# Kernel tuning notes

Hardware: AMD Instinct MI355X
Metric: run time of the kernel (lower is better)

Reference implementation:

```python
import jax, jax.numpy as jnp
import numpy as np

N_NODES = 20000
N_EDGES = 320000
IN_CH = 64
OUT_CH = 128

def _gat(x, src, dst, W, a_src, a_dst, bias, concat):
    # PyG GATConv: linear -> per-edge leaky_relu attention logits -> segment softmax over dst -> scatter-weighted sum
    N = x.shape[0]
    H, C = a_src.shape
    xl = (x @ W).reshape(N, H, C)                       # [N,H,C]
    al = (xl * a_src).sum(-1)                           # [N,H] src logits
    ar = (xl * a_dst).sum(-1)                           # [N,H] dst logits
    e = jax.nn.leaky_relu(al[src] + ar[dst], 0.2)       # [E,H]
    emax = jax.ops.segment_max(e, dst, num_segments=N)  # every node has a self loop -> no empty segments
    ee = jnp.exp(e - emax[dst])
    denom = jax.ops.segment_sum(ee, dst, num_segments=N)
    alpha = ee / (denom[dst] + 1e-16)                   # [E,H]
    out = jax.ops.segment_sum(xl[src] * alpha[:, :, None], dst, num_segments=N)  # [N,H,C]
    out = out.reshape(N, H * C) if concat else out.mean(axis=1)
    return out + bias

def setup_inputs() -> dict:
    key = jax.random.key(0)
    ks = jax.random.split(key, 32)
    def lin(k, fi, fo):
        return jax.random.normal(k, (fi, fo), jnp.float32) / np.sqrt(fi)
    def att(k, H, C):
        return jax.random.normal(k, (H, C), jnp.float32) / np.sqrt(C)
    x = jax.random.normal(ks[0], (N_NODES, IN_CH), jnp.float32)
    src = jax.random.randint(ks[1], (N_EDGES,), 0, N_NODES, jnp.int32)
    dst = jax.random.randint(ks[2], (N_EDGES,), 0, N_NODES, jnp.int32)
    dst = jnp.where(dst == src, (dst + 1) % N_NODES, dst)  # avoid pre-existing self loops
    edge_index = jnp.stack([src, dst])
    edge_time = jax.random.uniform(ks[3], (N_EDGES,), jnp.float32)
    H = 4
    return {
        "x": x, "edge_time": edge_time,
        "W1": lin(ks[4], IN_CH, 512), "as1": att(ks[5], H, 128), "ad1": att(ks[6], H, 128), "b1": jnp.zeros((512,), jnp.float32),
        "W2": lin(ks[7], 512, 512),   "as2": att(ks[8], H, 128), "ad2": att(ks[9], H, 128), "b2": jnp.zeros((512,), jnp.float32),
        "W3": lin(ks[10], 512, 512),  "as3": att(ks[11], H, 128), "ad3": att(ks[12], H, 128), "b3": jnp.zeros((OUT_CH,), jnp.float32),
        "tW1": lin(ks[13], 1, 64), "tb1": jnp.zeros((64,), jnp.float32),
        "tW2": lin(ks[14], 64, OUT_CH), "tb2": jnp.zeros((OUT_CH,), jnp.float32),
        "fW1": lin(ks[15], 2 * OUT_CH, OUT_CH), "fb1": jnp.zeros((OUT_CH,), jnp.float32),
        "fW2": lin(ks[16], OUT_CH, OUT_CH), "fb2": jnp.zeros((OUT_CH,), jnp.float32),
        "ln_g": jnp.ones((OUT_CH,), jnp.float32), "ln_b": jnp.zeros((OUT_CH,), jnp.float32),
        "rW": lin(ks[17], IN_CH, OUT_CH), "rb": jnp.zeros((OUT_CH,), jnp.float32),
        "edge_index": edge_index,
    }

def reference(x, edge_time, W1, as1, ad1, b1, W2, as2, ad2, b2, W3, as3, ad3, b3,
              tW1, tb1, tW2, tb2, fW1, fb1, fW2, fb2, ln_g, ln_b, rW, rb, edge_index):
    N = x.shape[0]
    loop = jnp.arange(N, dtype=edge_index.dtype)
    src = jnp.concatenate([edge_index[0], loop])
    dst = jnp.concatenate([edge_index[1], loop])
    # temporal embedding of raw (pre-self-loop) edges
    t = edge_time[:, None]
    time_emb = jax.nn.relu(t @ tW1 + tb1) @ tW2 + tb2    # [E, OUT_CH]
    x_res = x @ rW + rb
    h = jax.nn.relu(_gat(x, src, dst, W1, as1, ad1, b1, True))
    h = jax.nn.relu(_gat(h, src, dst, W2, as2, ad2, b2, True))
    h = jax.nn.relu(_gat(h, src, dst, W3, as3, ad3, b3, False))
    # x_agg[row] += h[col]  with (row, col) = (src, dst) incl. self loops
    agg = jax.ops.segment_sum(h[dst], src, num_segments=N)
    tm = jnp.broadcast_to(time_emb.mean(axis=0)[None, :], (N, time_emb.shape[1]))
    z = jnp.concatenate([agg, tm], axis=1)
    z = jax.nn.relu(z @ fW1 + fb1)                        # dropout is identity in eval
    z = z @ fW2 + fb2
    mu = z.mean(-1, keepdims=True)
    var = ((z - mu) ** 2).mean(-1, keepdims=True)
    z = (z - mu) / jnp.sqrt(var + 1e-5) * ln_g + ln_b
    return z + x_res
```

## Files before the change

kernel.cpp:

```cpp
#include <hip/hip_runtime.h>
#include <hip/hip_bf16.h>
#include <math.h>

typedef short bf16x8 __attribute__((ext_vector_type(8)));
typedef float f32x4 __attribute__((ext_vector_type(4)));

__device__ __forceinline__ float lrelu(float v) { return v > 0.f ? v : 0.2f * v; }

__device__ __forceinline__ void gload16(const void* g, void* l) {
  __builtin_amdgcn_global_load_lds(
      (const __attribute__((address_space(1))) void*)g,
      (__attribute__((address_space(3))) void*)l, 16, 0, 0);
}

__device__ __forceinline__ uint packbf(float v0, float v1) {
  __hip_bfloat16 h0 = __float2bfloat16(v0);
  __hip_bfloat16 h1 = __float2bfloat16(v1);
  return (uint)(*(unsigned short*)&h0) | ((uint)(*(unsigned short*)&h1) << 16);
}

struct PrepArgs {
  const float* W[6]; __hip_bfloat16* Wt[6]; int K[6]; int Nw[6]; int tstart[6];
  int NC, XB;
};

__global__ __launch_bounds__(256) void k_build(
    const int* __restrict__ src, const int* __restrict__ dst, int E,
    int* cntD, int* cntS,
    const float* __restrict__ et, const float* __restrict__ tW1,
    const float* __restrict__ tb1, float* __restrict__ tacc,
    PrepArgs a, const float* __restrict__ x,
    __hip_bfloat16* __restrict__ xbf, __hip_bfloat16* __restrict__ habf,
    __hip_bfloat16* __restrict__ aggbf, int N, int Mp, int EB) {
  __shared__ float se[256];
  __shared__ float buf[256];
  __shared__ float tile[32][65];
  int t = threadIdx.x;
  int bid = blockIdx.x;
  if (bid < EB) {
    int e = bid * 256 + t;
    if (e < E) {
      atomicAdd(&cntD[dst[e]], 1);
      atomicAdd(&cntS[src[e]], 1);
    }
    if (bid < 256) {
      int l = t & 63, w = t >> 6;
      float wk = tW1[l], bk = tb1[l];
      float a0 = 0.f, a1 = 0.f, a2 = 0.f, a3 = 0.f;
      for (int base = bid * 256; base < E; base += 256 * 256) {
        int idx = base + t;
        se[t] = (idx < E) ? et[idx] : 0.f;
        __syncthreads();
        int cnt = E - base; if (cnt > 256) cnt = 256;
        int s0 = w * 64;
        int c = cnt - s0; if (c < 0) c = 0; if (c > 64) c = 64;
        int j = 0;
        for (; j + 4 <= c; j += 4) {
          a0 += fmaxf(se[s0 + j] * wk + bk, 0.f);
          a1 += fmaxf(se[s0 + j + 1] * wk + bk, 0.f);
          a2 += fmaxf(se[s0 + j + 2] * wk + bk, 0.f);
          a3 += fmaxf(se[s0 + j + 3] * wk + bk, 0.f);
        }
        for (; j < c; ++j) a0 += fmaxf(se[s0 + j] * wk + bk, 0.f);
        __syncthreads();
      }
      buf[t] = (a0 + a1) + (a2 + a3);
      __syncthreads();
      if (t < 64) {
        float s = buf[t] + buf[t + 64] + buf[t + 128] + buf[t + 192];
        atomicAdd(&tacc[t], s);
      }
    }
    return;
  }
  int pbid = bid - EB;
  if (pbid < a.NC) {
    int m = 0;
#pragma unroll
    for (int i = 1; i < 6; ++i) if (pbid >= a.tstart[i]) m = i;
    const float* W = a.W[m];
    __hip_bfloat16* Wt = a.Wt[m];
    int K = a.K[m], Nw = a.Nw[m];
    int lt = pbid - a.tstart[m];
    int ntn = Nw >> 6;
    int bk = (lt / ntn) * 32, bn = (lt % ntn) * 64;
    int rn = t & 63, rk = t >> 6;
#pragma unroll
    for (int i = 0; i < 8; ++i)
      tile[rk + i * 4][rn] = W[(size_t)(bk + rk + i * 4) * Nw + bn + rn];
    __syncthreads();
    int wk2 = (t & 15) * 2, wn = t >> 4;
    uint* Wo = (uint*)Wt;
#pragma unroll
    for (int i = 0; i < 4; ++i) {
      int n = wn + i * 16;
      Wo[((size_t)(bn + n) * K + bk + wk2) >> 1] = packbf(tile[wk2][n], tile[wk2 + 1][n]);
    }
  } else if (pbid < a.NC + a.XB) {
    int i4 = (pbid - a.NC) * 256 + t;
    int row = i4 >> 4;
    float4 v = make_float4(0.f, 0.f, 0.f, 0.f);
    if (row < N) v = ((const float4*)x)[i4];
    uint2 p; p.x = packbf(v.x, v.y); p.y = packbf(v.z, v.w);
    ((uint2*)xbf)[i4] = p;
  } else {
    int row = N + (pbid - a.NC - a.XB);
    ((uint*)habf)[(size_t)row * 256 + t] = 0;
    if (t < 64) ((uint*)aggbf)[(size_t)row * 64 + t] = 0;
  }
}

__global__ __launch_bounds__(1024) void k_scan2c(const int* __restrict__ cntD, int* __restrict__ offD,
    const int* __restrict__ cntS, int* __restrict__ offS, int n,
    const float* __restrict__ tacc, const float* __restrict__ tW2,
    const float* __restrict__ tb2, const float* __restrict__ fW1,
    const float* __restrict__ fb1, float* __restrict__ cvec, int E) {
  int t = threadIdx.x;
  if (blockIdx.x == 2) {
    __shared__ float tm[128];
    if (t < 128) {
      float inv = 1.f / (float)E;
      float acc = tb2[t];
      for (int k = 0; k < 64; ++k) acc += (tacc[k] * inv) * tW2[k * 128 + t];
      tm[t] = acc;
    }
    __syncthreads();
    if (t < 128) {
      float c = fb1[t];
      for (int k = 0; k < 128; ++k) c += tm[k] * fW1[(128 + k) * 128 + t];
      cvec[t] = c;
    }
    return;
  }
  const int* cnt = blockIdx.x ? cntS : cntD;
  int* off = blockIdx.x ? offS : offD;
  __shared__ int sums[1024];
  int PT = (n + 1023) >> 10;
  int start = t * PT;
  int local = 0;
  for (int i = 0; i < PT; ++i) {
    int idx = start + i;
    if (idx < n) local += cnt[idx];
  }
  sums[t] = local;
  __syncthreads();
  for (int o = 1; o < 1024; o <<= 1) {
    int v = (t >= o) ? sums[t - o] : 0;
    __syncthreads();
    sums[t] += v;
    __syncthreads();
  }
  int run = sums[t] - local;
  for (int i = 0; i < PT; ++i) {
    int idx = start + i;
    if (idx < n) { off[idx] = run; run += cnt[idx]; }
  }
  if (t == 1023) off[n] = run;
}

__global__ __launch_bounds__(256) void gemm_e1(
    const __hip_bfloat16* __restrict__ A, const __hip_bfloat16* __restrict__ Bt,
    void* __restrict__ Cout, int M, int Nn, int K,
    const float* __restrict__ asrc, const float* __restrict__ adst,
    float* __restrict__ al, float* __restrict__ ar,
    float* __restrict__ C2, const float* __restrict__ bias2,
    int TBx,
    const int* __restrict__ fsrc, const int* __restrict__ fdst, int fE,
    const int* __restrict__ foffD, int* fcurD, int* flstD,
    const int* __restrict__ foffS, int* fcurS, int* flstS)
{
  __shared__ short As0[128 * 32];
  __shared__ short As1[128 * 32];
  __shared__ short Bs0[128 * 32];
  __shared__ short Bs1[128 * 32];
  if ((int)blockIdx.x >= TBx) {
    if (blockIdx.y == 0) {
      int e = ((int)blockIdx.x - TBx) * 256 + (int)threadIdx.x;
      if (e < fE) {
        int d = fdst[e], s = fsrc[e];
        int p = atomicAdd(&fcurD[d], 1);
        flstD[foffD[d] + p] = s;
        int q = atomicAdd(&fcurS[s], 1);
        flstS[foffS[s] + q] = d;
      }
    }
    return;
  }
  int tid = threadIdx.x;
  int bm = blockIdx.x * 128;
  int cb = blockIdx.y;
  int bn = cb * 128;
  int w = tid >> 6, l = tid & 63;
  int wr = (w >> 1) * 64, wc = (w & 1) * 64;
  f32x4 acc[4][4] = {};
  const short* Ag = (const short*)A;
  const short* Bg = (const short*)Bt;

  for (int k0 = 0; k0 < K; k0 += 64) {
#pragma unroll
    for (int i = 0; i < 2; ++i) {
      int slot = i * 256 + tid;
      int row = slot >> 2;
      int col = (slot & 3) * 8;
      const short* Arow = Ag + (size_t)(bm + row) * K + k0 + col;
      const short* Brow = Bg + (size_t)(bn + row) * K + k0 + col;
      gload16(Arow, &As0[slot * 8]);
      gload16(Arow + 32, &As1[slot * 8]);
      gload16(Brow, &Bs0[slot * 8]);
      gload16(Brow + 32, &Bs1[slot * 8]);
    }
    __syncthreads();
    {
      bf16x8 af[4], bfr[4];
#pragma unroll
      for (int m = 0; m < 4; ++m)
        af[m] = *(const bf16x8*)&As0[(wr + m * 16 + (l & 15)) * 32 + (l >> 4) * 8];
#pragma unroll
      for (int n = 0; n < 4; ++n)
        bfr[n] = *(const bf16x8*)&Bs0[(wc + n * 16 + (l & 15)) * 32 + (l >> 4) * 8];
#pragma unroll
      for (int m = 0; m < 4; ++m)
#pragma unroll
        for (int n = 0; n < 4; ++n)
          acc[m][n] = __builtin_amdgcn_mfma_f32_16x16x32_bf16(af[m], bfr[n], acc[m][n], 0, 0, 0);
    }
    {
      bf16x8 af[4], bfr[4];
#pragma unroll
      for (int m = 0; m < 4; ++m)
        af[m] = *(const bf16x8*)&As1[(wr + m * 16 + (l & 15)) * 32 + (l >> 4) * 8];
#pragma unroll
      for (int n = 0; n < 4; ++n)
        bfr[n] = *(const bf16x8*)&Bs1[(wc + n * 16 + (l & 15)) * 32 + (l >> 4) * 8];
#pragma unroll
      for (int m = 0; m < 4; ++m)
#pragma unroll
        for (int n = 0; n < 4; ++n)
          acc[m][n] = __builtin_amdgcn_mfma_f32_16x16x32_bf16(af[m], bfr[n], acc[m][n], 0, 0, 0);
    }
    __syncthreads();
  }

  int g = l >> 4, cc = l & 15, cr = g * 4;

  if (cb < 4) {
#pragma unroll
    for (int n = 0; n < 4; ++n) {
      int col = bn + wc + n * 16 + cc;
#pragma unroll
      for (int m = 0; m < 4; ++m) {
#pragma unroll
        for (int r = 0; r < 4; ++r) {
          int gm = bm + wr + m * 16 + cr + r;
          if (gm < M)
            ((__hip_bfloat16*)Cout)[(size_t)gm * 512 + col] = __float2bfloat16(acc[m][n][r]);
        }
      }
    }
    float asv[4], adv[4];
#pragma unroll
    for (int n = 0; n < 4; ++n) {
      int ch = bn + wc + n * 16 + cc;
      asv[n] = asrc[ch]; adv[n] = adst[ch];
    }
    float* spal = (float*)As0;
    float* spar = spal + 256;
#pragma unroll
    for (int m = 0; m < 4; ++m) {
#pragma unroll
      for (int r = 0; r < 4; ++r) {
        float pa = acc[m][0][r] * asv[0] + acc[m][1][r] * asv[1]
                 + acc[m][2][r] * asv[2] + acc[m][3][r] * asv[3];
        float pb = acc[m][0][r] * adv[0] + acc[m][1][r] * adv[1]
                 + acc[m][2][r] * adv[2] + acc[m][3][r] * adv[3];
#pragma unroll
        for (int o = 1; o < 16; o <<= 1) {
          pa += __shfl_xor(pa, o);
          pb += __shfl_xor(pb, o);
        }
        if (cc == 0) {
          int rl = m * 16 + cr + r;
          spal[w * 64 + rl] = pa;
          spar[w * 64 + rl] = pb;
        }
      }
    }
    __syncthreads();
    if ((w & 1) == 0) {
      float av = spal[w * 64 + l] + spal[(w + 1) * 64 + l];
      float rv = spar[w * 64 + l] + spar[(w + 1) * 64 + l];
      int row = bm + wr + l;
      if (row < Nn) { al[row * 4 + cb] = av; ar[row * 4 + cb] = rv; }
    }
  } else {
#pragma unroll
    for (int n = 0; n < 4; ++n) {
      int col2 = wc + n * 16 + cc;
      float bb = bias2[col2];
#pragma unroll
      for (int m = 0; m < 4; ++m) {
#pragma unroll
        for (int r = 0; r < 4; ++r) {
          int gm = bm + wr + m * 16 + cr + r;
          if (gm < Nn) C2[(size_t)gm * 128 + col2] = acc[m][n][r] + bb;
        }
      }
    }
  }
}

__global__ __launch_bounds__(256) void gemm_ff(
    const __hip_bfloat16* __restrict__ A, const __hip_bfloat16* __restrict__ B1t,
    const __hip_bfloat16* __restrict__ B2t, const float* __restrict__ cvec,
    const float* __restrict__ fb2, const float* __restrict__ lng,
    const float* __restrict__ lnb, float* __restrict__ resid, int M)
{
  __shared__ char ldsraw[32768 + 128 * 136 * 2];
  short* As0 = (short*)ldsraw;
  short* As1 = As0 + 4096;
  short* Bs0 = As1 + 4096;
  short* Bs1 = Bs0 + 4096;
  short* z1s = (short*)(ldsraw + 32768);
  int tid = threadIdx.x;
  int bm = blockIdx.x * 128;
  int w = tid >> 6, l = tid & 63;
  int wr = (w >> 1) * 64, wc = (w & 1) * 64;
  int g = l >> 4, cc = l & 15, cr = g * 4;
  const short* Ag = (const short*)A;
  const short* B1 = (const short*)B1t;
  const short* B2 = (const short*)B2t;
  f32x4 acc[4][4] = {};

  for (int k0 = 0; k0 < 128; k0 += 64) {
#pragma unroll
    for (int i = 0; i < 2; ++i) {
      int slot = i * 256 + tid;
      int row = slot >> 2;
      int col = (slot & 3) * 8;
      const short* Arow = Ag + (size_t)(bm + row) * 128 + k0 + col;
      const short* Brow = B1 + (size_t)row * 128 + k0 + col;
      gload16(Arow, &As0[slot * 8]);
      gload16(Arow + 32, &As1[slot * 8]);
      gload16(Brow, &Bs0[slot * 8]);
      gload16(Brow + 32, &Bs1[slot * 8]);
    }
    __syncthreads();
    {
      bf16x8 af[4], bfr[4];
#pragma unroll
      for (int m = 0; m < 4; ++m)
        af[m] = *(const bf16x8*)&As0[(wr + m * 16 + (l & 15)) * 32 + (l >> 4) * 8];
#pragma unroll
      for (int n = 0; n < 4; ++n)
        bfr[n] = *(const bf16x8*)&Bs0[(wc + n * 16 + (l & 15)) * 32 + (l >> 4) * 8];
#pragma unroll
      for (int m = 0; m < 4; ++m)
#pragma unroll
        for (int n = 0; n < 4; ++n)
          acc[m][n] = __builtin_amdgcn_mfma_f32_16x16x32_bf16(af[m], bfr[n], acc[m][n], 0, 0, 0);
    }
    {
      bf16x8 af[4], bfr[4];
#pragma unroll
      for (int m = 0; m < 4; ++m)
        af[m] = *(const bf16x8*)&As1[(wr + m * 16 + (l & 15)) * 32 + (l >> 4) * 8];
#pragma unroll
      for (int n = 0; n < 4; ++n)
        bfr[n] = *(const bf16x8*)&Bs1[(wc + n * 16 + (l & 15)) * 32 + (l >> 4) * 8];
#pragma unroll
      for (int m = 0; m < 4; ++m)
#pragma unroll
        for (int n = 0; n < 4; ++n)
          acc[m][n] = __builtin_amdgcn_mfma_f32_16x16x32_bf16(af[m], bfr[n], acc[m][n], 0, 0, 0);
    }
    __syncthreads();
  }

#pragma unroll
  for (int n = 0; n < 4; ++n) {
    int col = wc + n * 16 + cc;
    float bb = cvec[col];
#pragma unroll
    for (int m = 0; m < 4; ++m) {
#pragma unroll
      for (int r = 0; r < 4; ++r) {
        int rl = wr + m * 16 + cr + r;
        float v = fmaxf(acc[m][n][r] + bb, 0.f);
        __hip_bfloat16 hb = __float2bfloat16(v);
        z1s[rl * 136 + col] = *(short*)&hb;
      }
    }
  }
#pragma unroll
  for (int m = 0; m < 4; ++m)
#pragma unroll
    for (int n = 0; n < 4; ++n)
      acc[m][n] = (f32x4){0.f, 0.f, 0.f, 0.f};
  __syncthreads();

  for (int k0 = 0; k0 < 128; k0 += 64) {
#pragma unroll
    for (int i = 0; i < 2; ++i) {
      int slot = i * 256 + tid;
      int row = slot >> 2;
      int col = (slot & 3) * 8;
      const short* Brow = B2 + (size_t)row * 128 + k0 + col;
      gload16(Brow, &Bs0[slot * 8]);
      gload16(Brow + 32, &Bs1[slot * 8]);
    }
    __syncthreads();
    {
      bf16x8 af[4], bfr[4];
#pragma unroll
      for (int m = 0; m < 4; ++m)
        af[m] = *(const bf16x8*)&z1s[(wr + m * 16 + (l & 15)) * 136 + k0 + (l >> 4) * 8];
#pragma unroll
      for (int n = 0; n < 4; ++n)
        bfr[n] = *(const bf16x8*)&Bs0[(wc + n * 16 + (l & 15)) * 32 + (l >> 4) * 8];
#pragma unroll
      for (int m = 0; m < 4; ++m)
#pragma unroll
        for (int n = 0; n < 4; ++n)
          acc[m][n] = __builtin_amdgcn_mfma_f32_16x16x32_bf16(af[m], bfr[n], acc[m][n], 0, 0, 0);
    }
    {
      bf16x8 af[4], bfr[4];
#pragma unroll
      for (int m = 0; m < 4; ++m)
        af[m] = *(const bf16x8*)&z1s[(wr + m * 16 + (l & 15)) * 136 + k0 + 32 + (l >> 4) * 8];
#pragma unroll
      for (int n = 0; n < 4; ++n)
        bfr[n] = *(const bf16x8*)&Bs1[(wc + n * 16 + (l & 15)) * 32 + (l >> 4) * 8];
#pragma unroll
      for (int m = 0; m < 4; ++m)
#pragma unroll
        for (int n = 0; n < 4; ++n)
          acc[m][n] = __builtin_amdgcn_mfma_f32_16x16x32_bf16(af[m], bfr[n], acc[m][n], 0, 0, 0);
    }
    __syncthreads();
  }

  float bb[4], gl_[4], gb_[4];
#pragma unroll
  for (int n = 0; n < 4; ++n) {
    int col = wc + n * 16 + cc;
    bb[n] = fb2[col]; gl_[n] = lng[col]; gb_[n] = lnb[col];
  }
  float* ssum = (float*)As0;
  float* ssq = ssum + 256;
  float* smu = ssum + 512;
  float* srs = ssum + 640;
#pragma unroll
  for (int m = 0; m < 4; ++m) {
#pragma unroll
    for (int r = 0; r < 4; ++r) {
      float s = 0.f, q = 0.f;
#pragma unroll
      for (int n = 0; n < 4; ++n) {
        float z = acc[m][n][r] + bb[n];
        s += z; q += z * z;
      }
#pragma unroll
      for (int o = 1; o < 16; o <<= 1) {
        s += __shfl_xor(s, o);
        q += __shfl_xor(q, o);
      }
      if (cc == 0) {
        int rl = m * 16 + cr + r;
        ssum[w * 64 + rl] = s;
        ssq[w * 64 + rl] = q;
      }
    }
  }
  __syncthreads();
  if ((w & 1) == 0) {
    float s = ssum[w * 64 + l] + ssum[(w + 1) * 64 + l];
    float q = ssq[w * 64 + l] + ssq[(w + 1) * 64 + l];
    float mu = s * (1.f / 128.f);
    float var = q * (1.f / 128.f) - mu * mu;
    smu[wr + l] = mu;
    srs[wr + l] = rsqrtf(var + 1e-5f);
  }
  __syncthreads();
#pragma unroll
  for (int m = 0; m < 4; ++m) {
#pragma unroll
    for (int r = 0; r < 4; ++r) {
      int rl = wr + m * 16 + cr + r;
      int gm = bm + rl;
      if (gm < M) {
        float mu = smu[rl], rs = srs[rl];
#pragma unroll
        for (int n = 0; n < 4; ++n) {
          int col = wc + n * 16 + cc;
          float z = acc[m][n][r] + bb[n];
          float y = (z - mu) * rs * gl_[n] + gb_[n] + resid[(size_t)gm * 128 + col];
          resid[(size_t)gm * 128 + col] = y;
        }
      }
    }
  }
}

__global__ __launch_bounds__(256) void k_gat_agg(
    const __hip_bfloat16* __restrict__ xl, const float* __restrict__ al,
    const float* __restrict__ ar, const int* __restrict__ off,
    const int* __restrict__ lst, const float* __restrict__ bias,
    __hip_bfloat16* __restrict__ outb, __hip_bfloat16* __restrict__ outh,
    int mode, int N)
{
  __shared__ int   sside[4][64];
  __shared__ float sebuf[4][4][68];
  int w = threadIdx.x >> 6, l = threadIdx.x & 63;
  int d = blockIdx.x * 4 + w;
  bool active = (d < N);
  int base = 0, deg = 0, tot = 0;
  float4 arv = make_float4(0.f, 0.f, 0.f, 0.f);
  if (active) {
    base = off[d]; deg = off[d + 1] - base; tot = deg + 1;
    arv = *(const float4*)(ar + 4 * d);
  }
  int hh = l >> 4;
  float facc[8] = {0.f, 0.f, 0.f, 0.f, 0.f, 0.f, 0.f, 0.f};
  float dn0 = 0.f, dn1 = 0.f, dn2 = 0.f, dn3 = 0.f;
  const uint4* xw = (const uint4*)xl;
  auto fma8 = [&](uint4 pv, float e) {
    facc[0] += e * __uint_as_float(pv.x << 16);
    facc[1] += e * __uint_as_float(pv.x & 0xffff0000u);
    facc[2] += e * __uint_as_float(pv.y << 16);
    facc[3] += e * __uint_as_float(pv.y & 0xffff0000u);
    facc[4] += e * __uint_as_float(pv.z << 16);
    facc[5] += e * __uint_as_float(pv.z & 0xffff0000u);
    facc[6] += e * __uint_as_float(pv.w << 16);
    facc[7] += e * __uint_as_float(pv.w & 0xffff0000u);
  };
  for (int cb = 0; cb < tot; cb += 64) {
    int j = cb + l;
    float e0 = 0.f, e1 = 0.f, e2 = 0.f, e3 = 0.f;
    int sid = 0;
    if (j < tot) {
      sid = (j == deg) ? d : lst[base + j];
      float4 av = *(const float4*)(al + 4 * sid);
      e0 = __expf(lrelu(av.x + arv.x));
      e1 = __expf(lrelu(av.y + arv.y));
      e2 = __expf(lrelu(av.z + arv.z));
      e3 = __expf(lrelu(av.w + arv.w));
      dn0 += e0; dn1 += e1; dn2 += e2; dn3 += e3;
    }
    sside[w][l] = sid;
    sebuf[w][0][l] = e0; sebuf[w][1][l] = e1;
    sebuf[w][2][l] = e2; sebuf[w][3][l] = e3;
    int cnt = tot - cb; if (cnt > 64) cnt = 64;
    int jj = 0;
    for (; jj + 4 <= cnt; jj += 4) {
      int s0 = sside[w][jj], s1 = sside[w][jj + 1];
      int s2 = sside[w][jj + 2], s3 = sside[w][jj + 3];
      float ea = sebuf[w][hh][jj], eb = sebuf[w][hh][jj + 1];
      float ec = sebuf[w][hh][jj + 2], ed = sebuf[w][hh][jj + 3];
      uint4 p0 = xw[(size_t)s0 * 64 + l];
      uint4 p1 = xw[(size_t)s1 * 64 + l];
      uint4 p2 = xw[(size_t)s2 * 64 + l];
      uint4 p3 = xw[(size_t)s3 * 64 + l];
      fma8(p0, ea); fma8(p1, eb); fma8(p2, ec); fma8(p3, ed);
    }
    for (; jj < cnt; ++jj) {
      int s0 = sside[w][jj];
      float ea = sebuf[w][hh][jj];
      uint4 p0 = xw[(size_t)s0 * 64 + l];
      fma8(p0, ea);
    }
  }
#pragma unroll
  for (int o = 1; o < 64; o <<= 1) {
    dn0 += __shfl_xor(dn0, o); dn1 += __shfl_xor(dn1, o);
    dn2 += __shfl_xor(dn2, o); dn3 += __shfl_xor(dn3, o);
  }
  if (!active) return;
  float dsel = hh == 0 ? dn0 : hh == 1 ? dn1 : hh == 2 ? dn2 : dn3;
  float rden = 1.f / dsel;
  if (mode == 0) {
    int c8 = l * 8;
    const float4* bp = (const float4*)(bias + c8);
    float4 b0 = bp[0], b1 = bp[1];
    float vb[8] = {b0.x, b0.y, b0.z, b0.w, b1.x, b1.y, b1.z, b1.w};
    uint4 o4; uint* po = (uint*)&o4;
#pragma unroll
    for (int i = 0; i < 4; ++i) {
      float v0 = fmaxf(facc[2*i]   * rden + vb[2*i],   0.f);
      float v1 = fmaxf(facc[2*i+1] * rden + vb[2*i+1], 0.f);
      po[i] = packbf(v0, v1);
    }
    ((uint4*)outb)[(size_t)d * 64 + l] = o4;
  } else {
#pragma unroll
    for (int i = 0; i < 8; ++i) {
      facc[i] *= rden;
      facc[i] += __shfl_xor(facc[i], 16);
      facc[i] += __shfl_xor(facc[i], 32);
    }
    if (l < 16) {
      int c = l * 8;
      const float4* bp = (const float4*)(bias + c);
      float4 b0 = bp[0], b1 = bp[1];
      float vb[8] = {b0.x, b0.y, b0.z, b0.w, b1.x, b1.y, b1.z, b1.w};
      uint4 o4; uint* po = (uint*)&o4;
#pragma unroll
      for (int i = 0; i < 4; ++i) {
        float v0 = fmaxf(facc[2*i]   * 0.25f + vb[2*i],   0.f);
        float v1 = fmaxf(facc[2*i+1] * 0.25f + vb[2*i+1], 0.f);
        po[i] = packbf(v0, v1);
      }
      ((uint4*)outh)[(size_t)d * 16 + l] = o4;
    }
  }
}

__global__ __launch_bounds__(256) void k_aggsrc(const __hip_bfloat16* __restrict__ h3,
    const int* __restrict__ off, const int* __restrict__ lst,
    __hip_bfloat16* __restrict__ out, int N) {
  int w = threadIdx.x >> 6, l = threadIdx.x & 63;
  int n = blockIdx.x * 4 + w;
  if (n >= N) return;
  const uint* hw = (const uint*)h3;
  uint pv = hw[(size_t)n * 64 + l];
  float a0 = __uint_as_float(pv << 16);
  float a1 = __uint_as_float(pv & 0xffff0000u);
  float b0 = 0.f, b1 = 0.f, c0 = 0.f, c1 = 0.f, d0 = 0.f, d1 = 0.f;
  int b = off[n], e = off[n + 1];
  int j = b;
  for (; j + 4 <= e; j += 4) {
    int s0 = lst[j], s1 = lst[j + 1], s2 = lst[j + 2], s3 = lst[j + 3];
    uint q0 = hw[(size_t)s0 * 64 + l];
    uint q1 = hw[(size_t)s1 * 64 + l];
    uint q2 = hw[(size_t)s2 * 64 + l];
    uint q3 = hw[(size_t)s3 * 64 + l];
    a0 += __uint_as_float(q0 << 16); a1 += __uint_as_float(q0 & 0xffff0000u);
    b0 += __uint_as_float(q1 << 16); b1 += __uint_as_float(q1 & 0xffff0000u);
    c0 += __uint_as_float(q2 << 16); c1 += __uint_as_float(q2 & 0xffff0000u);
    d0 += __uint_as_float(q3 << 16); d1 += __uint_as_float(q3 & 0xffff0000u);
  }
  for (; j < e; ++j) {
    uint q = hw[(size_t)lst[j] * 64 + l];
    a0 += __uint_as_float(q << 16);
    a1 += __uint_as_float(q & 0xffff0000u);
  }
  ((uint*)out)[(size_t)n * 64 + l] = packbf((a0 + b0) + (c0 + d0), (a1 + b1) + (c1 + d1));
}

extern "C" void kernel_launch(void* const* d_in, const int* in_sizes, int n_in,
                              void* d_out, int out_size, void* d_ws, size_t ws_size,
                              hipStream_t stream) {
  (void)n_in; (void)out_size; (void)ws_size;
  const float* x   = (const float*)d_in[0];
  const float* et  = (const float*)d_in[1];
  const float* W1  = (const float*)d_in[2];
  const float* as1 = (const float*)d_in[3];
  const float* ad1 = (const float*)d_in[4];
  const float* b1  = (const float*)d_in[5];
  const float* W2  = (const float*)d_in[6];
  const float* as2 = (const float*)d_in[7];
  const float* ad2 = (const float*)d_in[8];
  const float* b2  = (const float*)d_in[9];
  const float* W3  = (const float*)d_in[10];
  const float* as3 = (const float*)d_in[11];
  const float* ad3 = (const float*)d_in[12];
  const float* b3  = (const float*)d_in[13];
  const float* tW1 = (const float*)d_in[14];
  const float* tb1 = (const float*)d_in[15];
  const float* tW2 = (const float*)d_in[16];
  const float* tb2 = (const float*)d_in[17];
  const float* fW1 = (const float*)d_in[18];
  const float* fb1 = (const float*)d_in[19];
  const float* fW2 = (const float*)d_in[20];
  const float* fb2 = (const float*)d_in[21];
  const float* lng = (const float*)d_in[22];
  const float* lnb = (const float*)d_in[23];
  const float* rW  = (const float*)d_in[24];
  const float* rb  = (const float*)d_in[25];
  const int*   ei  = (const int*)d_in[26];
  const int N = in_sizes[0] / 64;
  const int E = in_sizes[26] / 2;
  const int Mp = ((N + 127) / 128) * 128;
  const int* src = ei;
  const int* dst = ei + E;

  char* cur = (char*)d_ws;
  auto carve = [&](size_t bytes) { char* p = cur; cur += (bytes + 255) & ~(size_t)255; return p; };
  __hip_bfloat16* xbf  = (__hip_bfloat16*)carve((size_t)Mp * 64 * 2);
  __hip_bfloat16* habf = (__hip_bfloat16*)carve((size_t)Mp * 512 * 2);
  __hip_bfloat16* xlbf = (__hip_bfloat16*)carve((size_t)Mp * 512 * 2);
  __hip_bfloat16* wtCat= (__hip_bfloat16*)carve((size_t)640 * 64 * 2);
  __hip_bfloat16* wt2  = (__hip_bfloat16*)carve((size_t)512 * 512 * 2);
  __hip_bfloat16* wt3  = (__hip_bfloat16*)carve((size_t)512 * 512 * 2);
  __hip_bfloat16* wtF1 = (__hip_bfloat16*)carve((size_t)128 * 128 * 2);
  __hip_bfloat16* wtF2 = (__hip_bfloat16*)carve((size_t)128 * 128 * 2);
  __hip_bfloat16* aggbf= (__hip_bfloat16*)carve((size_t)Mp * 128 * 2);
  __hip_bfloat16* h3   = (__hip_bfloat16*)carve((size_t)N * 128 * 2);
  float* al   = (float*)carve((size_t)N * 4 * 4);
  float* ar   = (float*)carve((size_t)N * 4 * 4);
  float* cvec = (float*)carve(128 * 4);
  int* offD = (int*)carve((size_t)(N + 1) * 4);
  int* offS = (int*)carve((size_t)(N + 1) * 4);
  int* lstD = (int*)carve((size_t)E * 4);
  int* lstS = (int*)carve((size_t)E * 4);
  char* zstart = cur;
  int* cntD = (int*)carve((size_t)N * 4);
  int* curD = (int*)carve((size_t)N * 4);
  int* cntS = (int*)carve((size_t)N * 4);
  int* curS = (int*)carve((size_t)N * 4);
  float* tacc = (float*)carve(64 * 4);
  size_t zbytes = (size_t)(cur - zstart);
  float* xres = (float*)d_out;

  hipMemsetAsync(zstart, 0, zbytes, stream);

  const int EB = (E + 255) / 256;
  PrepArgs pa;
  {
    int ts = 0;
    auto setd = [&](int i, const float* W, __hip_bfloat16* Wt, int K, int Nw) {
      pa.W[i] = W; pa.Wt[i] = Wt; pa.K[i] = K; pa.Nw[i] = Nw; pa.tstart[i] = ts;
      ts += (K / 32) * (Nw / 64);
    };
    setd(0, W1, wtCat, 64, 512);
    setd(1, W2, wt2, 512, 512);
    setd(2, W3, wt3, 512, 512);
    setd(3, rW, wtCat + (size_t)512 * 64, 64, 128);
    setd(4, fW1, wtF1, 128, 128);
    setd(5, fW2, wtF2, 128, 128);
    pa.NC = ts;
    pa.XB = Mp / 16;
    int grid = EB + pa.NC + pa.XB + (Mp - N);
    k_build<<<grid, 256, 0, stream>>>(src, dst, E, cntD, cntS, et, tW1, tb1, tacc,
                                      pa, x, xbf, habf, aggbf, N, Mp, EB);
  }
  k_scan2c<<<3, 1024, 0, stream>>>(cntD, offD, cntS, offS, N, tacc, tW2, tb2, fW1, fb1, cvec, E);

  const int TB = Mp / 128;
  const int GB = (N + 3) / 4;
  const int BIG = 1 << 30;

  gemm_e1<<<dim3(TB + EB, 5), 256, 0, stream>>>(xbf, wtCat, xlbf, Mp, N, 64,
      as1, ad1, al, ar, xres, rb,
      TB, src, dst, E, offD, curD, lstD, offS, curS, lstS);
  k_gat_agg<<<GB, 256, 0, stream>>>(xlbf, al, ar, offD, lstD, b1, habf, nullptr, 0, N);
  gemm_e1<<<dim3(TB, 4), 256, 0, stream>>>(habf, wt2, xlbf, Mp, N, 512,
      as2, ad2, al, ar, nullptr, nullptr,
      BIG, nullptr, nullptr, 0, nullptr, nullptr, nullptr, nullptr, nullptr, nullptr);
  k_gat_agg<<<GB, 256, 0, stream>>>(xlbf, al, ar, offD, lstD, b2, habf, nullptr, 0, N);
  gemm_e1<<<dim3(TB, 4), 256, 0, stream>>>(habf, wt3, xlbf, Mp, N, 512,
      as3, ad3, al, ar, nullptr, nullptr,
      BIG, nullptr, nullptr, 0, nullptr, nullptr, nullptr, nullptr, nullptr, nullptr);
  k_gat_agg<<<GB, 256, 0, stream>>>(xlbf, al, ar, offD, lstD, b3, nullptr, h3, 1, N);

  k_aggsrc<<<GB, 256, 0, stream>>>(h3, offS, lstS, aggbf, N);

  gemm_ff<<<TB, 256, 0, stream>>>(aggbf, wtF1, wtF2, cvec, fb2, lng, lnb, xres, N);
}
```

Baseline: 368.0 us.

## Record per-edge slots during counting to remove atomics from CSR fill

The edge-counting pass now keeps counts in 8 separate copies (chosen by block index) and saves each edge's atomicAdd return value as its slot. The scan produces per-copy offsets, so the fill step writes each edge straight to offset+slot instead of doing a second round of atomics on cursor arrays. This trades the fill-phase atomics and some counting contention for extra slot and offset arrays, more memory traffic, and an 8x larger zeroed count region and scan read. Neighbor order within each node's list is now fixed by copy index and slot.

Measured after the change: 487.4 us. 1.32x slower.

```diff
diff --git a/kernel.cpp b/kernel.cpp
--- a/kernel.cpp
+++ b/kernel.cpp
@@ -26,7 +26,7 @@
 
 __global__ __launch_bounds__(256) void k_build(
     const int* __restrict__ src, const int* __restrict__ dst, int E,
-    int* cntD, int* cntS,
+    int* cntD, int* cntS, int* slotD, int* slotS,
     const float* __restrict__ et, const float* __restrict__ tW1,
     const float* __restrict__ tb1, float* __restrict__ tacc,
     PrepArgs a, const float* __restrict__ x,
@@ -40,8 +40,10 @@
   if (bid < EB) {
     int e = bid * 256 + t;
     if (e < E) {
-      atomicAdd(&cntD[dst[e]], 1);
-      atomicAdd(&cntS[src[e]], 1);
+      int d = dst[e], s = src[e];
+      int c = bid & 7;
+      slotD[e] = atomicAdd(&cntD[c * N + d], 1);
+      slotS[e] = atomicAdd(&cntS[c * N + s], 1);
     }
     if (bid < 256) {
       int l = t & 63, w = t >> 6;
@@ -53,15 +55,15 @@
         __syncthreads();
         int cnt = E - base; if (cnt > 256) cnt = 256;
         int s0 = w * 64;
-        int c = cnt - s0; if (c < 0) c = 0; if (c > 64) c = 64;
+        int c2 = cnt - s0; if (c2 < 0) c2 = 0; if (c2 > 64) c2 = 64;
         int j = 0;
-        for (; j + 4 <= c; j += 4) {
+        for (; j + 4 <= c2; j += 4) {
           a0 += fmaxf(se[s0 + j] * wk + bk, 0.f);
           a1 += fmaxf(se[s0 + j + 1] * wk + bk, 0.f);
           a2 += fmaxf(se[s0 + j + 2] * wk + bk, 0.f);
           a3 += fmaxf(se[s0 + j + 3] * wk + bk, 0.f);
         }
-        for (; j < c; ++j) a0 += fmaxf(se[s0 + j] * wk + bk, 0.f);
+        for (; j < c2; ++j) a0 += fmaxf(se[s0 + j] * wk + bk, 0.f);
         __syncthreads();
       }
       buf[t] = (a0 + a1) + (a2 + a3);
@@ -110,8 +112,10 @@
   }
 }
 
-__global__ __launch_bounds__(1024) void k_scan2c(const int* __restrict__ cntD, int* __restrict__ offD,
-    const int* __restrict__ cntS, int* __restrict__ offS, int n,
+__global__ __launch_bounds__(1024) void k_scan2c(
+    const int* __restrict__ cntD, int* __restrict__ offD, int* __restrict__ coffD,
+    const int* __restrict__ cntS, int* __restrict__ offS, int* __restrict__ coffS,
+    int n,
     const float* __restrict__ tacc, const float* __restrict__ tW2,
     const float* __restrict__ tb2, const float* __restrict__ fW1,
     const float* __restrict__ fb1, float* __restrict__ cvec, int E) {
@@ -134,13 +138,17 @@
   }
   const int* cnt = blockIdx.x ? cntS : cntD;
   int* off = blockIdx.x ? offS : offD;
+  int* coff = blockIdx.x ? coffS : coffD;
   __shared__ int sums[1024];
   int PT = (n + 1023) >> 10;
   int start = t * PT;
   int local = 0;
   for (int i = 0; i < PT; ++i) {
     int idx = start + i;
-    if (idx < n) local += cnt[idx];
+    if (idx < n) {
+#pragma unroll
+      for (int c = 0; c < 8; ++c) local += cnt[c * n + idx];
+    }
   }
   sums[t] = local;
   __syncthreads();
@@ -153,7 +161,17 @@
   int run = sums[t] - local;
   for (int i = 0; i < PT; ++i) {
     int idx = start + i;
-    if (idx < n) { off[idx] = run; run += cnt[idx]; }
+    if (idx < n) {
+      off[idx] = run;
+      int acc = run;
+#pragma unroll
+      for (int c = 0; c < 8; ++c) {
+        int v = cnt[c * n + idx];
+        coff[c * n + idx] = acc;
+        acc += v;
+      }
+      run = acc;
+    }
   }
   if (t == 1023) off[n] = run;
 }
@@ -166,8 +184,8 @@
     float* __restrict__ C2, const float* __restrict__ bias2,
     int TBx,
     const int* __restrict__ fsrc, const int* __restrict__ fdst, int fE,
-    const int* __restrict__ foffD, int* fcurD, int* flstD,
-    const int* __restrict__ foffS, int* fcurS, int* flstS)
+    const int* __restrict__ fcoffD, const int* __restrict__ fslotD, int* flstD,
+    const int* __restrict__ fcoffS, const int* __restrict__ fslotS, int* flstS)
 {
   __shared__ short As0[128 * 32];
   __shared__ short As1[128 * 32];
@@ -178,10 +196,9 @@
       int e = ((int)blockIdx.x - TBx) * 256 + (int)threadIdx.x;
       if (e < fE) {
         int d = fdst[e], s = fsrc[e];
-        int p = atomicAdd(&fcurD[d], 1);
-        flstD[foffD[d] + p] = s;
-        int q = atomicAdd(&fcurS[s], 1);
-        flstS[foffS[s] + q] = d;
+        int c = (e >> 8) & 7;
+        flstD[fcoffD[c * Nn + d] + fslotD[e]] = s;
+        flstS[fcoffS[c * Nn + s] + fslotS[e]] = d;
       }
     }
     return;
@@ -703,11 +720,13 @@
   int* offS = (int*)carve((size_t)(N + 1) * 4);
   int* lstD = (int*)carve((size_t)E * 4);
   int* lstS = (int*)carve((size_t)E * 4);
+  int* slotD = (int*)carve((size_t)E * 4);
+  int* slotS = (int*)carve((size_t)E * 4);
+  int* coffD = (int*)carve((size_t)8 * N * 4);
+  int* coffS = (int*)carve((size_t)8 * N * 4);
   char* zstart = cur;
-  int* cntD = (int*)carve((size_t)N * 4);
-  int* curD = (int*)carve((size_t)N * 4);
-  int* cntS = (int*)carve((size_t)N * 4);
-  int* curS = (int*)carve((size_t)N * 4);
+  int* cntD = (int*)carve((size_t)8 * N * 4);
+  int* cntS = (int*)carve((size_t)8 * N * 4);
   float* tacc = (float*)carve(64 * 4);
   size_t zbytes = (size_t)(cur - zstart);
   float* xres = (float*)d_out;
@@ -731,10 +750,12 @@
     pa.NC = ts;
     pa.XB = Mp / 16;
     int grid = EB + pa.NC + pa.XB + (Mp - N);
-    k_build<<<grid, 256, 0, stream>>>(src, dst, E, cntD, cntS, et, tW1, tb1, tacc,
+    k_build<<<grid, 256, 0, stream>>>(src, dst, E, cntD, cntS, slotD, slotS,
+                                      et, tW1, tb1, tacc,
                                       pa, x, xbf, habf, aggbf, N, Mp, EB);
   }
-  k_scan2c<<<3, 1024, 0, stream>>>(cntD, offD, cntS, offS, N, tacc, tW2, tb2, fW1, fb1, cvec, E);
+  k_scan2c<<<3, 1024, 0, stream>>>(cntD, offD, coffD, cntS, offS, coffS, N,
+                                   tacc, tW2, tb2, fW1, fb1, cvec, E);
 
   const int TB = Mp / 128;
   const int GB = (N + 3) / 4;
@@ -742,7 +763,7 @@
 
   gemm_e1<<<dim3(TB + EB, 5), 256, 0, stream>>>(xbf, wtCat, xlbf, Mp, N, 64,
       as1, ad1, al, ar, xres, rb,
-      TB, src, dst, E, offD, curD, lstD, offS, curS, lstS);
+      TB, src, dst, E, coffD, slotD, lstD, coffS, slotS, lstS);
   k_gat_agg<<<GB, 256, 0, stream>>>(xlbf, al, ar, offD, lstD, b1, habf, nullptr, 0, N);
   gemm_e1<<<dim3(TB, 4), 256, 0, stream>>>(habf, wt2, xlbf, Mp, N, 512,
       as2, ad2, al, ar, nullptr, nullptr,
```
